# Performance work log

Measured on AMD Instinct MI355X. Metric: run time of the kernel, lower is better.

Reference implementation:

```python
import jax, jax.numpy as jnp
import numpy as np

UNITS = 512
WINDOW = 2


def causal_conv1d(x, w, b):
    # x: (B, T, D), w: (W, D, U), b: (U,) -> (B, T, U), causal (left) padding
    y = jax.lax.conv_general_dilated(
        x, w, window_strides=(1,), padding=[(w.shape[0] - 1, 0)],
        dimension_numbers=("NWC", "WIO", "NWC"))
    return y + b


def setup_inputs() -> dict:
    key = jax.random.key(0)
    ks = jax.random.split(key, 7)
    B, T, D, U, W = 16, 4096, 512, UNITS, WINDOW
    scale = (2.0 / (W * D + U)) ** 0.5  # glorot-ish
    x = jax.random.normal(ks[0], (B, T, D), dtype=jnp.float32)
    Wz = jax.random.normal(ks[1], (W, D, U), dtype=jnp.float32) * scale
    bz = jnp.zeros((U,), dtype=jnp.float32)
    Wf = jax.random.normal(ks[2], (W, D, U), dtype=jnp.float32) * scale
    bf = jnp.zeros((U,), dtype=jnp.float32)
    Wo = jax.random.normal(ks[3], (W, D, U), dtype=jnp.float32) * scale
    bo = jnp.zeros((U,), dtype=jnp.float32)
    return {"x": x, "Wz": Wz, "bz": bz, "Wf": Wf, "bf": bf, "Wo": Wo, "bo": bo}


def reference(x, Wz, bz, Wf, bf, Wo, bo):
    # Gate projections via causal conv1d
    z = jnp.tanh(causal_conv1d(x, Wz, bz))          # candidate (B,T,U)
    f = jax.nn.sigmoid(causal_conv1d(x, Wf, bf))    # forget gate
    o = jax.nn.sigmoid(causal_conv1d(x, Wo, bo))    # output gate

    # Linear recurrence h_t = f_t * h_{t-1} + (1 - f_t) * z_t, h_0 = 0,
    # computed as a parallel associative scan over affine maps (a, b):
    # h -> a*h + b, composition (a1,b1) then (a2,b2) = (a2*a1, a2*b1 + b2).
    a = f
    b = (1.0 - f) * z

    def combine(c1, c2):
        a1, b1 = c1
        a2, b2 = c2
        return a2 * a1, a2 * b1 + b2

    _, h = jax.lax.associative_scan(combine, (a, b), axis=1)
    return o * h  # (B, T, U), return_sequences=True
```

## Files before the change

kernel.cpp:

```cpp
#include <hip/hip_runtime.h>
#include <cstdio>
#include <cstdint>

#define B_  16
#define T_  4096
#define D_  512
#define U_  512
#define KK  1024
#define M_  (B_*T_)
#define NTOT 1536

#define CHUNK 128
#define NCH   (T_/CHUNK)

typedef __attribute__((ext_vector_type(8))) short  bf16x8;
typedef __attribute__((ext_vector_type(4))) float  f32x4;
typedef __attribute__((ext_vector_type(8))) unsigned short u16x8;

__device__ __forceinline__ unsigned short f2bf(float f) {
    unsigned int u = __float_as_uint(f);
    unsigned int r = (u + 0x7fffu + ((u >> 16) & 1u)) >> 16;
    return (unsigned short)r;
}

__device__ __forceinline__ void gl_lds16(const void* g, void* l) {
    __builtin_amdgcn_global_load_lds(
        (const __attribute__((address_space(1))) void*)g,
        (__attribute__((address_space(3))) void*)l, 16, 0, 0);
}

__global__ __launch_bounds__(256)
void convert_x_kernel(const float* __restrict__ x, unsigned short* __restrict__ xz)
{
    const size_t e = ((size_t)blockIdx.x * 256 + threadIdx.x) * 8;
    const size_t row = e >> 9;
    const int    d   = (int)(e & 511);
    const int    tz  = (int)(row % 4097);
    const size_t b   = row / 4097;
    u16x8 o;
    if (tz == 0) {
        #pragma unroll
        for (int i = 0; i < 8; ++i) o[i] = 0;
    } else {
        const size_t src = (((b << 12) + (size_t)(tz - 1)) << 9) + d;
        const float4 v0 = *reinterpret_cast<const float4*>(x + src);
        const float4 v1 = *reinterpret_cast<const float4*>(x + src + 4);
        o[0] = f2bf(v0.x); o[1] = f2bf(v0.y); o[2] = f2bf(v0.z); o[3] = f2bf(v0.w);
        o[4] = f2bf(v1.x); o[5] = f2bf(v1.y); o[6] = f2bf(v1.z); o[7] = f2bf(v1.w);
    }
    *reinterpret_cast<u16x8*>(xz + e) = o;
}

__global__ __launch_bounds__(256)
void convert_wt_kernel(const float* __restrict__ Wz, const float* __restrict__ Wf,
                       const float* __restrict__ Wo, unsigned short* __restrict__ Wt)
{
    __shared__ float tile[32][33];
    const int g = blockIdx.z;
    const float* __restrict__ W = (g == 0) ? Wz : (g == 1 ? Wf : Wo);
    const int k0 = blockIdx.x * 32;
    const int u0 = blockIdx.y * 32;
    const int tx = threadIdx.x, ty = threadIdx.y;
    #pragma unroll
    for (int r = 0; r < 4; ++r)
        tile[ty + r * 8][tx] = W[(size_t)(k0 + ty + r * 8) * 512 + u0 + tx];
    __syncthreads();
    #pragma unroll
    for (int r = 0; r < 4; ++r) {
        const int u = u0 + ty + r * 8;
        Wt[(size_t)(g * 512 + u) * 1024 + k0 + tx] = f2bf(tile[tx][ty + r * 8]);
    }
}

__global__ __launch_bounds__(512, 2)
void gemm_mfma_kernel(const unsigned short* __restrict__ xz,
                      const unsigned short* __restrict__ Wt,
                      const float* __restrict__ bz, const float* __restrict__ bfg,
                      const float* __restrict__ bo,
                      float* __restrict__ zbuf, float* __restrict__ fbuf,
                      float* __restrict__ obuf)
{
    __shared__ unsigned short As[2 * 256 * 64];
    __shared__ unsigned short Bs[2 * 256 * 64];

    const int tid  = threadIdx.x;
    const int lane = tid & 63;
    const int wave = tid >> 6;
    const int wu   = wave & 3;
    const int wm   = wave >> 2;

    const int flat  = blockIdx.x;
    const int xcd   = flat & 7;
    const int idx   = flat >> 3;
    const int ntile = idx % 6;
    const int mt    = xcd * 32 + idx / 6;
    const int m0 = mt * 256;
    const int n0 = ntile * 256;
    const int b  = m0 >> 12;
    const int t0 = m0 & 4095;

    const int srow = wave * 8 + (lane >> 3);
    const int swz  = (lane & 7) ^ (lane >> 3);
    const unsigned short* gA = xz + ((size_t)(b * 4097 + t0 + srow) << 9) + swz * 8;
    const unsigned short* gB = Wt + ((size_t)(n0 + srow) << 10) + swz * 8;
    char* AsB = (char*)As;
    char* BsB = (char*)Bs;
    const int ldst = wave * 1024;

    auto STAGE = [&](int kt, int bf) {
        #pragma unroll
        for (int i = 0; i < 4; ++i)
            gl_lds16(gA + i * 32768 + kt * 64, AsB + bf * 32768 + i * 8192 + ldst);
        #pragma unroll
        for (int i = 0; i < 4; ++i)
            gl_lds16(gB + i * 65536 + kt * 64, BsB + bf * 32768 + i * 8192 + ldst);
    };

    f32x4 acc[4][8];
    #pragma unroll
    for (int i = 0; i < 4; ++i)
        #pragma unroll
        for (int j = 0; j < 8; ++j)
            acc[i][j] = (f32x4){0.f, 0.f, 0.f, 0.f};

    const int l15 = lane & 15;
    const int ck0 = (((lane >> 4) + 0) ^ (lane & 7)) * 16;
    const int ck1 = (((lane >> 4) + 4) ^ (lane & 7)) * 16;
    const int wvBase = (wu * 64 + l15) * 128;
    const int xvBase = (wm * 128 + l15) * 128;

    auto COMPUTE = [&](int bf) {
        const char* AB = AsB + bf * 32768;
        const char* BB = BsB + bf * 32768;
        bf16x8 wv[4][2];
        #pragma unroll
        for (int i = 0; i < 4; ++i) {
            wv[i][0] = *reinterpret_cast<const bf16x8*>(BB + wvBase + i * 2048 + ck0);
            wv[i][1] = *reinterpret_cast<const bf16x8*>(BB + wvBase + i * 2048 + ck1);
        }
        #pragma unroll
        for (int jh = 0; jh < 2; ++jh) {
            bf16x8 xv[4][2];
            #pragma unroll
            for (int j2 = 0; j2 < 4; ++j2) {
                xv[j2][0] = *reinterpret_cast<const bf16x8*>(
                    AB + xvBase + (jh * 4 + j2) * 2048 + ck0);
                xv[j2][1] = *reinterpret_cast<const bf16x8*>(
                    AB + xvBase + (jh * 4 + j2) * 2048 + ck1);
            }
            __builtin_amdgcn_s_setprio(1);
            #pragma unroll
            for (int i = 0; i < 4; ++i)
                #pragma unroll
                for (int j2 = 0; j2 < 4; ++j2) {
                    acc[i][jh * 4 + j2] = __builtin_amdgcn_mfma_f32_16x16x32_bf16(
                        wv[i][0], xv[j2][0], acc[i][jh * 4 + j2], 0, 0, 0);
                    acc[i][jh * 4 + j2] = __builtin_amdgcn_mfma_f32_16x16x32_bf16(
                        wv[i][1], xv[j2][1], acc[i][jh * 4 + j2], 0, 0, 0);
                }
            __builtin_amdgcn_s_setprio(0);
        }
    };

    STAGE(0, 0);
    STAGE(1, 1);

    #pragma unroll 1
    for (int t = 0; t < 15; ++t) {
        asm volatile("s_waitcnt vmcnt(8)" ::: "memory");
        __builtin_amdgcn_s_barrier();
        asm volatile("" ::: "memory");
        COMPUTE(t & 1);
        asm volatile("" ::: "memory");
        __builtin_amdgcn_s_barrier();
        asm volatile("" ::: "memory");
        if (t < 14) STAGE(t + 2, t & 1);
    }
    asm volatile("s_waitcnt vmcnt(0)" ::: "memory");
    __builtin_amdgcn_s_barrier();
    asm volatile("" ::: "memory");
    COMPUTE(1);

    const int gate = ntile >> 1;
    float* __restrict__ outg = (gate == 0) ? zbuf : (gate == 1 ? fbuf : obuf);
    const float* __restrict__ bg = (gate == 0) ? bz : (gate == 1 ? bfg : bo);
    const int ubase = (ntile & 1) * 256 + wu * 64 + ((lane >> 4) << 2);
    const int mbase = m0 + wm * 128 + l15;

    #pragma unroll
    for (int i = 0; i < 4; ++i) {
        const int u = ubase + i * 16;
        const float4 b4 = *reinterpret_cast<const float4*>(bg + u);
        #pragma unroll
        for (int j = 0; j < 8; ++j) {
            const int m = mbase + j * 16;
            float4 v;
            v.x = acc[i][j][0] + b4.x;
            v.y = acc[i][j][1] + b4.y;
            v.z = acc[i][j][2] + b4.z;
            v.w = acc[i][j][3] + b4.w;
            if (gate == 0) {
                v.x = 2.0f / (1.0f + __expf(-2.0f * v.x)) - 1.0f;
                v.y = 2.0f / (1.0f + __expf(-2.0f * v.y)) - 1.0f;
                v.z = 2.0f / (1.0f + __expf(-2.0f * v.z)) - 1.0f;
                v.w = 2.0f / (1.0f + __expf(-2.0f * v.w)) - 1.0f;
            } else {
                v.x = 1.0f / (1.0f + __expf(-v.x));
                v.y = 1.0f / (1.0f + __expf(-v.y));
                v.z = 1.0f / (1.0f + __expf(-v.z));
                v.w = 1.0f / (1.0f + __expf(-v.w));
            }
            *reinterpret_cast<float4*>(outg + (size_t)m * 512 + u) = v;
        }
    }
}

__global__ __launch_bounds__(256)
void chunk_summary_kernel(const float* __restrict__ fbuf,
                          const float* __restrict__ zbuf,
                          float* __restrict__ Ach, float* __restrict__ Bch)
{
    const int bc = blockIdx.x;
    const int c  = bc & (NCH - 1);
    const int b  = bc >> 5;
    const int u  = threadIdx.x * 2;

    const long long base = ((long long)(b * T_ + c * CHUNK)) * U_ + u;
    float2 A = make_float2(1.0f, 1.0f);
    float2 Bv = make_float2(0.0f, 0.0f);
    #pragma unroll 8
    for (int i = 0; i < CHUNK; ++i) {
        const float2 f = *reinterpret_cast<const float2*>(fbuf + base + (long long)i * U_);
        const float2 z = *reinterpret_cast<const float2*>(zbuf + base + (long long)i * U_);
        Bv.x = f.x * Bv.x + (1.0f - f.x) * z.x;
        Bv.y = f.y * Bv.y + (1.0f - f.y) * z.y;
        A.x *= f.x;
        A.y *= f.y;
    }
    const int idx = (b * NCH + c) * U_ + u;
    *reinterpret_cast<float2*>(Ach + idx) = A;
    *reinterpret_cast<float2*>(Bch + idx) = Bv;
}

__global__ __launch_bounds__(256)
void chunk_prefix_kernel(const float* __restrict__ Ach,
                         const float* __restrict__ Bch,
                         float* __restrict__ Hin)
{
    const int g = blockIdx.x * 256 + threadIdx.x;
    const int b = g >> 8;
    const int u = (g & 255) * 2;
    float2 h = make_float2(0.0f, 0.0f);
    #pragma unroll 4
    for (int c = 0; c < NCH; ++c) {
        const int idx = (b * NCH + c) * U_ + u;
        *reinterpret_cast<float2*>(Hin + idx) = h;
        const float2 A = *reinterpret_cast<const float2*>(Ach + idx);
        const float2 Bv = *reinterpret_cast<const float2*>(Bch + idx);
        h.x = A.x * h.x + Bv.x;
        h.y = A.y * h.y + Bv.y;
    }
}

__global__ __launch_bounds__(256)
void scan_apply_kernel(const float* __restrict__ fbuf,
                       const float* __restrict__ zbuf,
                       const float* __restrict__ obuf,
                       const float* __restrict__ Hin,
                       float* __restrict__ out)
{
    const int bc = blockIdx.x;
    const int c  = bc & (NCH - 1);
    const int b  = bc >> 5;
    const int u  = threadIdx.x * 2;

    const long long base = ((long long)(b * T_ + c * CHUNK)) * U_ + u;
    float2 h = *reinterpret_cast<const float2*>(Hin + (b * NCH + c) * U_ + u);
    #pragma unroll 8
    for (int i = 0; i < CHUNK; ++i) {
        const long long p = base + (long long)i * U_;
        const float2 f = *reinterpret_cast<const float2*>(fbuf + p);
        const float2 z = *reinterpret_cast<const float2*>(zbuf + p);
        const float2 o = *reinterpret_cast<const float2*>(obuf + p);
        h.x = f.x * h.x + (1.0f - f.x) * z.x;
        h.y = f.y * h.y + (1.0f - f.y) * z.y;
        float2 r;
        r.x = o.x * h.x;
        r.y = o.y * h.y;
        *reinterpret_cast<float2*>(out + p) = r;
    }
}

extern "C" void kernel_launch(void* const* d_in, const int* in_sizes, int n_in,
                              void* d_out, int out_size, void* d_ws, size_t ws_size,
                              hipStream_t stream)
{
    const float* x  = (const float*)d_in[0];
    const float* Wz = (const float*)d_in[1];
    const float* bz = (const float*)d_in[2];
    const float* Wf = (const float*)d_in[3];
    const float* bf = (const float*)d_in[4];
    const float* Wo = (const float*)d_in[5];
    const float* bo = (const float*)d_in[6];
    float* out = (float*)d_out;

    const size_t S  = (size_t)M_ * U_;
    const size_t Sc = (size_t)B_ * NCH * U_;
    const size_t XZ = (size_t)B_ * (T_ + 1) * D_;
    const size_t WT = (size_t)NTOT * KK;

    float* zbuf = (float*)d_ws;
    float* fbuf = zbuf + S;
    float* obuf = fbuf + S;
    unsigned short* xz = (unsigned short*)(obuf + S);
    unsigned short* Wt = xz + XZ;
    float* Ach = (float*)(Wt + WT);
    float* Bch = Ach + Sc;
    float* Hin = Bch + Sc;

    const size_t need = 3 * S * sizeof(float) + (XZ + WT) * sizeof(unsigned short)
                      + 3 * Sc * sizeof(float);
    if (ws_size < need) {
        fprintf(stderr, "QRNN kernel: ws_size=%zu < needed %zu bytes!\n",
                ws_size, need);
    }

    {
        const size_t nthreads = XZ / 8;
        convert_x_kernel<<<dim3((unsigned)(nthreads / 256)), 256, 0, stream>>>(x, xz);
        convert_wt_kernel<<<dim3(32, 16, 3), dim3(32, 8), 0, stream>>>(Wz, Wf, Wo, Wt);
    }
    gemm_mfma_kernel<<<dim3(6 * (M_ / 256)), 512, 0, stream>>>(
        xz, Wt, bz, bf, bo, zbuf, fbuf, obuf);
    chunk_summary_kernel<<<dim3(B_ * NCH), 256, 0, stream>>>(fbuf, zbuf, Ach, Bch);
    chunk_prefix_kernel<<<dim3(16), 256, 0, stream>>>(Ach, Bch, Hin);
    scan_apply_kernel<<<dim3(B_ * NCH), 256, 0, stream>>>(fbuf, zbuf, obuf, Hin, out);
}
```

Before: 668.0 us.

## Switch GEMM to a 4-stage K=32 LDS ring with one barrier per step

```diff
diff --git a/kernel.cpp b/kernel.cpp
--- a/kernel.cpp
+++ b/kernel.cpp
@@ -72,7 +72,7 @@
     }
 }
 
-__global__ __launch_bounds__(512, 2)
+__global__ __launch_bounds__(512, 1)
 void gemm_mfma_kernel(const unsigned short* __restrict__ xz,
                       const unsigned short* __restrict__ Wt,
                       const float* __restrict__ bz, const float* __restrict__ bfg,
@@ -80,8 +80,8 @@
                       float* __restrict__ zbuf, float* __restrict__ fbuf,
                       float* __restrict__ obuf)
 {
-    __shared__ unsigned short As[2 * 256 * 64];
-    __shared__ unsigned short Bs[2 * 256 * 64];
+    __shared__ unsigned short lds[4 * 16384];
+    char* L = (char*)lds;
 
     const int tid  = threadIdx.x;
     const int lane = tid & 63;
@@ -99,21 +99,27 @@
     const int b  = m0 >> 12;
     const int t0 = m0 & 4095;
 
-    const int srow = wave * 8 + (lane >> 3);
-    const int swz  = (lane & 7) ^ (lane >> 3);
-    const unsigned short* gA = xz + ((size_t)(b * 4097 + t0 + srow) << 9) + swz * 8;
-    const unsigned short* gB = Wt + ((size_t)(n0 + srow) << 10) + swz * 8;
-    char* AsB = (char*)As;
-    char* BsB = (char*)Bs;
-    const int ldst = wave * 1024;
-
-    auto STAGE = [&](int kt, int bf) {
-        #pragma unroll
-        for (int i = 0; i < 4; ++i)
-            gl_lds16(gA + i * 32768 + kt * 64, AsB + bf * 32768 + i * 8192 + ldst);
-        #pragma unroll
-        for (int i = 0; i < 4; ++i)
-            gl_lds16(gB + i * 65536 + kt * 64, BsB + bf * 32768 + i * 8192 + ldst);
+    const unsigned short* srcA[2];
+    const unsigned short* srcB[2];
+    #pragma unroll
+    for (int l = 0; l < 2; ++l) {
+        const int g  = l * 512 + tid;
+        const int pr = g >> 3, p = g & 7;
+        const int e  = p ^ (pr & 7);
+        const int r  = pr * 2 + (e >> 2);
+        const int c  = e & 3;
+        srcA[l] = xz + ((size_t)(b * 4097 + t0 + r) << 9) + c * 8;
+        srcB[l] = Wt + ((size_t)(n0 + r) << 10) + c * 8;
+    }
+    const int dstOff = tid * 16;
+
+    auto STAGE = [&](int tau) {
+        char* s = L + (tau & 3) * 32768;
+        const int ko = tau * 32;
+        gl_lds16(srcA[0] + ko, s + dstOff);
+        gl_lds16(srcA[1] + ko, s + 8192  + dstOff);
+        gl_lds16(srcB[0] + ko, s + 16384 + dstOff);
+        gl_lds16(srcB[1] + ko, s + 24576 + dstOff);
     };
 
     f32x4 acc[4][8];
@@ -123,64 +129,50 @@
         for (int j = 0; j < 8; ++j)
             acc[i][j] = (f32x4){0.f, 0.f, 0.f, 0.f};
 
-    const int l15 = lane & 15;
-    const int ck0 = (((lane >> 4) + 0) ^ (lane & 7)) * 16;
-    const int ck1 = (((lane >> 4) + 4) ^ (lane & 7)) * 16;
-    const int wvBase = (wu * 64 + l15) * 128;
-    const int xvBase = (wm * 128 + l15) * 128;
-
-    auto COMPUTE = [&](int bf) {
-        const char* AB = AsB + bf * 32768;
-        const char* BB = BsB + bf * 32768;
-        bf16x8 wv[4][2];
-        #pragma unroll
-        for (int i = 0; i < 4; ++i) {
-            wv[i][0] = *reinterpret_cast<const bf16x8*>(BB + wvBase + i * 2048 + ck0);
-            wv[i][1] = *reinterpret_cast<const bf16x8*>(BB + wvBase + i * 2048 + ck1);
-        }
-        #pragma unroll
-        for (int jh = 0; jh < 2; ++jh) {
-            bf16x8 xv[4][2];
+    const int h     = (lane >> 1) & 7;
+    const int pos16 = ((((lane & 1) << 2) | (lane >> 4)) ^ h) << 4;
+    const int aBase = ((wm * 64 + h) << 7) + pos16;
+    const int bBase = 16384 + ((wu * 32 + h) << 7) + pos16;
+
+    auto COMPUTE = [&](int tau) {
+        const char* s = L + (tau & 3) * 32768;
+        bf16x8 wv[4], xv[8];
+        #pragma unroll
+        for (int i = 0; i < 4; ++i)
+            wv[i] = *reinterpret_cast<const bf16x8*>(s + bBase + i * 1024);
+        #pragma unroll
+        for (int j = 0; j < 8; ++j)
+            xv[j] = *reinterpret_cast<const bf16x8*>(s + aBase + j * 1024);
+        __builtin_amdgcn_s_setprio(1);
+        #pragma unroll
+        for (int i = 0; i < 4; ++i)
             #pragma unroll
-            for (int j2 = 0; j2 < 4; ++j2) {
-                xv[j2][0] = *reinterpret_cast<const bf16x8*>(
-                    AB + xvBase + (jh * 4 + j2) * 2048 + ck0);
-                xv[j2][1] = *reinterpret_cast<const bf16x8*>(
-                    AB + xvBase + (jh * 4 + j2) * 2048 + ck1);
-            }
-            __builtin_amdgcn_s_setprio(1);
-            #pragma unroll
-            for (int i = 0; i < 4; ++i)
-                #pragma unroll
-                for (int j2 = 0; j2 < 4; ++j2) {
-                    acc[i][jh * 4 + j2] = __builtin_amdgcn_mfma_f32_16x16x32_bf16(
-                        wv[i][0], xv[j2][0], acc[i][jh * 4 + j2], 0, 0, 0);
-                    acc[i][jh * 4 + j2] = __builtin_amdgcn_mfma_f32_16x16x32_bf16(
-                        wv[i][1], xv[j2][1], acc[i][jh * 4 + j2], 0, 0, 0);
-                }
-            __builtin_amdgcn_s_setprio(0);
-        }
+            for (int j = 0; j < 8; ++j)
+                acc[i][j] = __builtin_amdgcn_mfma_f32_16x16x32_bf16(
+                    wv[i], xv[j], acc[i][j], 0, 0, 0);
+        __builtin_amdgcn_s_setprio(0);
     };
 
-    STAGE(0, 0);
-    STAGE(1, 1);
+    STAGE(0); STAGE(1); STAGE(2);
 
     #pragma unroll 1
-    for (int t = 0; t < 15; ++t) {
+    for (int tau = 0; tau < 29; ++tau) {
         asm volatile("s_waitcnt vmcnt(8)" ::: "memory");
         __builtin_amdgcn_s_barrier();
-        asm volatile("" ::: "memory");
-        COMPUTE(t & 1);
-        asm volatile("" ::: "memory");
-        __builtin_amdgcn_s_barrier();
-        asm volatile("" ::: "memory");
-        if (t < 14) STAGE(t + 2, t & 1);
-    }
+        STAGE(tau + 3);
+        COMPUTE(tau);
+    }
+    asm volatile("s_waitcnt vmcnt(8)" ::: "memory");
+    __builtin_amdgcn_s_barrier();
+    COMPUTE(29);
+    asm volatile("s_waitcnt vmcnt(4)" ::: "memory");
+    __builtin_amdgcn_s_barrier();
+    COMPUTE(30);
     asm volatile("s_waitcnt vmcnt(0)" ::: "memory");
     __builtin_amdgcn_s_barrier();
-    asm volatile("" ::: "memory");
-    COMPUTE(1);
-
+    COMPUTE(31);
+
+    const int l15  = lane & 15;
     const int gate = ntile >> 1;
     float* __restrict__ outg = (gate == 0) ? zbuf : (gate == 1 ? fbuf : obuf);
     const float* __restrict__ bg = (gate == 0) ? bz : (gate == 1 ? bfg : bo);
```

Result: no change. 656.0 us (-1.8%).
